# Kernel optimization log

Hardware: AMD Instinct MI355X
Metric: run time of the kernel (lower is better)

## Reference

```python
import jax, jax.numpy as jnp
import numpy as np

B, S, DIM = 2, 2048, 1024
HID = 2048          # multiple_of-rounded hidden dim
E, NSH, TOPK = 8, 2, 2


def _ffn(x, w1, w2, w3):
    return (jax.nn.silu(x @ w1.T) * (x @ w3.T)) @ w2.T


def setup_inputs() -> dict:
    key = jax.random.key(0)
    ks = jax.random.split(key, 8)
    sc = 0.02  # init scale for stability
    return {
        "x": jax.random.normal(ks[0], (B, S, DIM), jnp.float32),
        "router_w": jax.random.normal(ks[1], (E, DIM), jnp.float32) * sc,
        "expert_bias": jnp.zeros((E,), jnp.float32),
        "w1": jax.random.normal(ks[2], (E, HID, DIM), jnp.float32) * sc,
        "w3": jax.random.normal(ks[3], (E, HID, DIM), jnp.float32) * sc,
        "w2": jax.random.normal(ks[4], (E, DIM, HID), jnp.float32) * sc,
        "sw1": jax.random.normal(ks[5], (NSH, HID, DIM), jnp.float32) * sc,
        "sw3": jax.random.normal(ks[6], (NSH, HID, DIM), jnp.float32) * sc,
        "sw2": jax.random.normal(ks[7], (NSH, DIM, HID), jnp.float32) * sc,
    }


def reference(x, router_w, expert_bias, w1, w3, w2, sw1, sw3, sw2):
    bs, sl, d = x.shape
    xf = x.reshape(-1, d)  # [T, d]

    # shared experts (always-on)
    shared = jnp.zeros_like(xf)
    for i in range(sw1.shape[0]):
        shared = shared + _ffn(xf, sw1[i], sw2[i], sw3[i])

    # router with aux-free load-balance bias
    logits = xf @ router_w.T + expert_bias  # [T, E]
    rw, sel = jax.lax.top_k(logits, TOPK)   # [T, K]
    rw = jax.nn.softmax(rw.astype(jnp.float32), axis=-1).astype(x.dtype)

    # combine weights per (token, expert): sum of routing weights over topk slots
    onehot = jax.nn.one_hot(sel, E, dtype=x.dtype)        # [T, K, E]
    combine = jnp.einsum('tk,tke->te', rw, onehot)        # [T, E]

    # per-expert FFN accumulated via scan (equivalent to gather-FFN-scatter)
    def body(acc, ew):
        e1, e3, e2, cw = ew  # cw: [T]
        acc = acc + cw[:, None] * _ffn(xf, e1, e2, e3)
        return acc, None

    out, _ = jax.lax.scan(body, jnp.zeros_like(xf), (w1, w3, w2, combine.T))
    out = out + shared
    return out.reshape(bs, sl, -1)
```

## Files before the change

### kernel.cpp

```cpp
#include <hip/hip_runtime.h>
#include <stdint.h>

#define T_TOK 4096
#define DIMD  1024
#define HIDN  2048
#define NEXP  8
#define RMAX  10240
#define RROWS (RMAX + 2 * T_TOK)

typedef float f32x4 __attribute__((ext_vector_type(4)));
typedef short s16x8 __attribute__((ext_vector_type(8)));

__device__ __forceinline__ uint16_t f2bf(float f) {
    uint32_t u = __builtin_bit_cast(uint32_t, f);
    u += 0x7fffu + ((u >> 16) & 1u);
    return (uint16_t)(u >> 16);
}
__device__ __forceinline__ float bf2f(uint32_t h) {
    return __builtin_bit_cast(float, h << 16);
}
__device__ __forceinline__ uint32_t pk2(float a, float b) {
    return (uint32_t)f2bf(a) | ((uint32_t)f2bf(b) << 16);
}
__device__ __forceinline__ int swz(int r, int cbyte) {
    return r * 128 + (cbyte ^ ((r & 7) << 4));
}
__device__ __forceinline__ void gload16(const void* g, void* l) {
    __builtin_amdgcn_global_load_lds(
        (const __attribute__((address_space(1))) void*)g,
        (__attribute__((address_space(3))) void*)l, 16, 0, 0);
}
#define BAR()        asm volatile("s_barrier" ::: "memory")
#define WAIT_VM4()   asm volatile("s_waitcnt vmcnt(4)" ::: "memory")
#define WAIT_VM0()   asm volatile("s_waitcnt vmcnt(0)" ::: "memory")
#define WAIT_LGKM0() asm volatile("s_waitcnt lgkmcnt(0)" ::: "memory")

__device__ __forceinline__ void stage128x64(const uint16_t* gbase, int ldk,
                                            char* lds, int wv, int lane) {
    #pragma unroll
    for (int i = 0; i < 4; ++i) {
        int s = (wv * 4 + i) * 64 + lane;
        int row = s >> 3;
        int cb = ((s & 7) << 4) ^ ((row & 7) << 4);
        gload16(gbase + (size_t)row * ldk + (cb >> 1), lds + ((wv * 4 + i) << 10));
    }
}


struct CvtArgs {
    const float* s[7];
    uint16_t*    d[7];
    int          nq[7];
    int          mode[7];
};

__global__ void cvt_all_kernel(CvtArgs a) {
    int base = blockIdx.x * blockDim.x + threadIdx.x;
    int stride = gridDim.x * blockDim.x;
    #pragma unroll
    for (int seg = 0; seg < 7; ++seg) {
        const float4* sp = (const float4*)a.s[seg];
        uint2* dp = (uint2*)a.d[seg];
        int n = a.nq[seg];
        int mode = a.mode[seg];
        for (int i = base; i < n; i += stride) {
            float4 v = sp[i];
            uint2 o; o.x = pk2(v.x, v.y); o.y = pk2(v.z, v.w);
            int di = i;
            if (mode) {
                int e = i >> 19;
                int rem = i & 524287;
                int nr = rem >> 8;
                int kq = rem & 255;
                int np = ((nr >> 4) << 5) + ((mode == 2) ? 16 : 0) + (nr & 15);
                di = (e << 20) + (np << 8) + kq;
            }
            dp[di] = o;
        }
    }
}

__global__ __launch_bounds__(256)
void router_kernel(const float* __restrict__ x, const float* __restrict__ rw,
                   const float* __restrict__ bias,
                   int* __restrict__ sel, float* __restrict__ wgt,
                   int* __restrict__ cnt) {
    __shared__ float rws[NEXP * DIMD];
    int tid = threadIdx.x;
    for (int i = tid; i < NEXP * DIMD / 4; i += 256)
        ((float4*)rws)[i] = ((const float4*)rw)[i];
    __syncthreads();

    int wid = tid >> 6, lane = tid & 63;
    float b[NEXP];
    #pragma unroll
    for (int e = 0; e < NEXP; ++e) b[e] = bias[e];

    int t0 = (blockIdx.x * 4 + wid) * 8;
    for (int j = 0; j < 8; ++j) {
        int t = t0 + j;
        const float4* xr = (const float4*)(x + (size_t)t * DIMD);
        float p[NEXP] = {};
        #pragma unroll
        for (int c = 0; c < 4; ++c) {
            float4 xv = xr[c * 64 + lane];
            #pragma unroll
            for (int e = 0; e < NEXP; ++e) {
                float4 wv = *(const float4*)(rws + e * DIMD + c * 256 + lane * 4);
                p[e] += xv.x * wv.x + xv.y * wv.y + xv.z * wv.z + xv.w * wv.w;
            }
        }
        #pragma unroll
        for (int off = 32; off >= 1; off >>= 1) {
            #pragma unroll
            for (int e = 0; e < NEXP; ++e) p[e] += __shfl_xor(p[e], off, 64);
        }
        if (lane == 0) {
            #pragma unroll
            for (int e = 0; e < NEXP; ++e) p[e] += b[e];
            float l0 = -1e30f; int i0 = 0;
            #pragma unroll
            for (int e = 0; e < NEXP; ++e) { if (p[e] > l0) { l0 = p[e]; i0 = e; } }
            float l1 = -1e30f; int i1 = 0;
            #pragma unroll
            for (int e = 0; e < NEXP; ++e) { if (e == i0) continue; if (p[e] > l1) { l1 = p[e]; i1 = e; } }
            float e1 = expf(l1 - l0);
            float d = 1.f + e1;
            sel[t * 2] = i0; sel[t * 2 + 1] = i1;
            wgt[t * 2] = 1.f / d; wgt[t * 2 + 1] = e1 / d;
            atomicAdd(&cnt[i0], 1);
            atomicAdd(&cnt[i1], 1);
        }
    }
}

__global__ void offs_kernel(const int* __restrict__ cnt, int* __restrict__ offs) {
    if (threadIdx.x == 0 && blockIdx.x == 0) {
        int o = 0;
        for (int e = 0; e < NEXP; ++e) { offs[e] = o; o += (cnt[e] + 255) & ~255; }
        offs[NEXP] = o;
    }
}

__global__ void assign_kernel(const int* __restrict__ sel, const int* __restrict__ offs,
                              int* __restrict__ fill, int* __restrict__ row_of,
                              int* __restrict__ tok) {
    int i = blockIdx.x * blockDim.x + threadIdx.x;
    if (i < 2 * T_TOK) {
        int e = sel[i];
        int r = offs[e] + atomicAdd(&fill[e], 1);
        row_of[i] = r;
        tok[r] = i >> 1;
    } else if (i < 4 * T_TOK) {
        int j = i - 2 * T_TOK;
        tok[offs[NEXP] + j] = j & (T_TOK - 1);
    }
}

__global__ void combine_kernel(const uint16_t* __restrict__ H2, const int* __restrict__ row_of,
                               const float* __restrict__ wgt, const int* __restrict__ offs,
                               float* __restrict__ out) {
    int t = blockIdx.x;
    int c = threadIdx.x * 8;
    int r0 = row_of[t * 2], r1 = row_of[t * 2 + 1];
    int s0 = offs[NEXP] + t, s1 = s0 + T_TOK;
    float w0 = wgt[t * 2], w1 = wgt[t * 2 + 1];
    uint4 a = *(const uint4*)(H2 + (size_t)r0 * DIMD + c);
    uint4 b = *(const uint4*)(H2 + (size_t)r1 * DIMD + c);
    uint4 u = *(const uint4*)(H2 + (size_t)s0 * DIMD + c);
    uint4 v = *(const uint4*)(H2 + (size_t)s1 * DIMD + c);
    float4 o0, o1;
    o0.x = w0 * bf2f(a.x & 0xffffu) + w1 * bf2f(b.x & 0xffffu) + bf2f(u.x & 0xffffu) + bf2f(v.x & 0xffffu);
    o0.y = w0 * bf2f(a.x >> 16)     + w1 * bf2f(b.x >> 16)     + bf2f(u.x >> 16)     + bf2f(v.x >> 16);
    o0.z = w0 * bf2f(a.y & 0xffffu) + w1 * bf2f(b.y & 0xffffu) + bf2f(u.y & 0xffffu) + bf2f(v.y & 0xffffu);
    o0.w = w0 * bf2f(a.y >> 16)     + w1 * bf2f(b.y >> 16)     + bf2f(u.y >> 16)     + bf2f(v.y >> 16);
    o1.x = w0 * bf2f(a.z & 0xffffu) + w1 * bf2f(b.z & 0xffffu) + bf2f(u.z & 0xffffu) + bf2f(v.z & 0xffffu);
    o1.y = w0 * bf2f(a.z >> 16)     + w1 * bf2f(b.z >> 16)     + bf2f(u.z >> 16)     + bf2f(v.z >> 16);
    o1.z = w0 * bf2f(a.w & 0xffffu) + w1 * bf2f(b.w & 0xffffu) + bf2f(u.w & 0xffffu) + bf2f(v.w & 0xffffu);
    o1.w = w0 * bf2f(a.w >> 16)     + w1 * bf2f(b.w >> 16)     + bf2f(u.w >> 16)     + bf2f(v.w >> 16);
    float* o = out + (size_t)t * DIMD + c;
    *(float4*)o = o0;
    *(float4*)(o + 4) = o1;
}

__global__ __launch_bounds__(512, 2)
void gemm13_8p(const uint16_t* __restrict__ A, const int* __restrict__ tok,
               const uint16_t* __restrict__ W, uint16_t* __restrict__ H,
               const int* __restrict__ offs) {
    constexpr int K = DIMD;
    constexpr int NT = K / 64;
    __shared__ __align__(16) char lds[131072];

    int row0 = blockIdx.y * 256;
    int rsh = row0 - offs[NEXP];
    int e;
    if (rsh >= 0) {
        if (rsh >= 2 * T_TOK) return;
        e = NEXP + (rsh >> 12);
    } else {
        e = 0;
        while (row0 >= offs[e + 1]) ++e;
    }
    const uint16_t* wp = W + (size_t)e * (4096ull * 1024ull);
    int col0 = blockIdx.x * 256;

    int tid = threadIdx.x, lane = tid & 63, wid = tid >> 6;
    int wm = wid >> 2, wn = wid & 3;

    int sslot = (lane & 3) ^ ((tid >> 3) & 3);
    uint32_t aoff[2], boff[2];
    #pragma unroll
    for (int i = 0; i < 2; ++i) {
        int r = i * 128 + (tid >> 2);
        int garow = tok[row0 + r];
        aoff[i] = (uint32_t)garow * K + sslot * 8;
        boff[i] = (uint32_t)(col0 + r) * K + sslot * 8;
    }
    int ldsw = wid * 1024;

    int rslot = (((lane >> 4) ^ ((lane >> 1) & 3)) << 4);
    int aro = (wm * 128 + (lane & 15)) * 64 + rslot;
    int bro = (wn * 64 + (lane & 15)) * 64 + rslot;

    #define STAGE_A(buf, kt, ks) { \
        gload16(A + aoff[0] + (kt) + (ks) * 32, (buf) + (ks) * 16384 + ldsw); \
        gload16(A + aoff[1] + (kt) + (ks) * 32, (buf) + (ks) * 16384 + 8192 + ldsw); }
    #define STAGE_B(buf, kt, ks) { \
        gload16(wp + boff[0] + (kt) + (ks) * 32, (buf) + 32768 + (ks) * 16384 + ldsw); \
        gload16(wp + boff[1] + (kt) + (ks) * 32, (buf) + 32768 + (ks) * 16384 + 8192 + ldsw); }

    STAGE_A(lds, 0, 0); STAGE_B(lds, 0, 0);
    STAGE_A(lds, 0, 1); STAGE_B(lds, 0, 1);
    WAIT_VM4();
    BAR();

    f32x4 acc[8][4] = {};

    for (int t = 0; t < NT; ++t) {
        char* cur = lds + (t & 1) * 65536;
        char* nxt = lds + ((t + 1) & 1) * 65536;
        int kt1 = (t + 1) * 64;
        bool pre = (t + 1 < NT);
        s16x8 av[4], bv[4], av2[4];

        #pragma unroll
        for (int f = 0; f < 4; ++f) av[f] = *(const s16x8*)(cur + aro + f * 1024);
        #pragma unroll
        for (int f = 0; f < 4; ++f) bv[f] = *(const s16x8*)(cur + 32768 + bro + f * 1024);
        if (pre) STAGE_A(nxt, kt1, 0);
        BAR(); WAIT_LGKM0();
        __builtin_amdgcn_s_setprio(1);
        #pragma unroll
        for (int j = 0; j < 4; ++j)
            #pragma unroll
            for (int i = 0; i < 4; ++i)
                acc[i][j] = __builtin_amdgcn_mfma_f32_16x16x32_bf16(av[i], bv[j], acc[i][j], 0, 0, 0);
        __builtin_amdgcn_s_setprio(0);
        BAR();

        #pragma unroll
        for (int f = 0; f < 4; ++f) av2[f] = *(const s16x8*)(cur + aro + (f + 4) * 1024);
        if (pre) STAGE_B(nxt, kt1, 0);
        BAR(); WAIT_LGKM0();
        __builtin_amdgcn_s_setprio(1);
        #pragma unroll
        for (int j = 0; j < 4; ++j)
            #pragma unroll
            for (int i = 0; i < 4; ++i)
                acc[i + 4][j] = __builtin_amdgcn_mfma_f32_16x16x32_bf16(av2[i], bv[j], acc[i + 4][j], 0, 0, 0);
        __builtin_amdgcn_s_setprio(0);
        if (pre) { WAIT_VM4(); } else { WAIT_VM0(); }
        BAR();

        #pragma unroll
        for (int f = 0; f < 4; ++f) av[f] = *(const s16x8*)(cur + 16384 + aro + f * 1024);
        #pragma unroll
        for (int f = 0; f < 4; ++f) bv[f] = *(const s16x8*)(cur + 32768 + 16384 + bro + f * 1024);
        if (pre) STAGE_A(nxt, kt1, 1);
        BAR(); WAIT_LGKM0();
        __builtin_amdgcn_s_setprio(1);
        #pragma unroll
        for (int j = 0; j < 4; ++j)
            #pragma unroll
            for (int i = 0; i < 4; ++i)
                acc[i][j] = __builtin_amdgcn_mfma_f32_16x16x32_bf16(av[i], bv[j], acc[i][j], 0, 0, 0);
        __builtin_amdgcn_s_setprio(0);
        BAR();

        #pragma unroll
        for (int f = 0; f < 4; ++f) av2[f] = *(const s16x8*)(cur + 16384 + aro + (f + 4) * 1024);
        if (pre) STAGE_B(nxt, kt1, 1);
        BAR(); WAIT_LGKM0();
        __builtin_amdgcn_s_setprio(1);
        #pragma unroll
        for (int j = 0; j < 4; ++j)
            #pragma unroll
            for (int i = 0; i < 4; ++i)
                acc[i + 4][j] = __builtin_amdgcn_mfma_f32_16x16x32_bf16(av2[i], bv[j], acc[i + 4][j], 0, 0, 0);
        __builtin_amdgcn_s_setprio(0);
        if (pre) WAIT_VM4();
        BAR();
    }
    #undef STAGE_A
    #undef STAGE_B

    #pragma unroll
    for (int i = 0; i < 8; ++i) {
        int row = row0 + wm * 128 + i * 16 + ((lane >> 4) << 2);
        #pragma unroll
        for (int m = 0; m < 2; ++m) {
            int hc = ((col0 + wn * 64) >> 1) + m * 16 + (lane & 15);
            #pragma unroll
            for (int rg = 0; rg < 4; ++rg) {
                float a1 = acc[i][2 * m][rg];
                float a3 = acc[i][2 * m + 1][rg];
                float hv = (a1 / (1.f + __expf(-a1))) * a3;
                H[(size_t)(row + rg) * HIDN + hc] = f2bf(hv);
            }
        }
    }
}

__global__ __launch_bounds__(256, 3)
void gemm2_kernel(const uint16_t* __restrict__ Hg,
                  const uint16_t* __restrict__ W2, uint16_t* __restrict__ H2,
                  const int* __restrict__ offs) {
    __shared__ __align__(16) char lds[32768];
    char* As = lds;
    char* Bs = lds + 16384;

    const int K = HIDN;
    int row0 = blockIdx.y * 128;
    int rsh = row0 - offs[NEXP];
    int e;
    if (rsh >= 0) {
        if (rsh >= 2 * T_TOK) return;
        e = NEXP + (rsh >> 12);
    } else {
        e = 0;
        while (row0 >= offs[e + 1]) ++e;
    }
    const uint16_t* b2 = W2 + (size_t)e * DIMD * HIDN;
    int col0 = blockIdx.x * 128;

    int tid = threadIdx.x, lane = tid & 63;
    int wv = tid >> 6, wm = wv >> 1, wn = wv & 1;

    f32x4 acc[4][4] = {};

    for (int kt = 0; kt < K; kt += 64) {
        __syncthreads();
        stage128x64(Hg + (size_t)row0 * K + kt, K, As, wv, lane);
        stage128x64(b2 + (size_t)col0 * K + kt, K, Bs, wv, lane);
        __syncthreads();

        #pragma unroll
        for (int s = 0; s < 2; ++s) {
            int cb = s * 64 + ((lane >> 4) << 4);
            s16x8 av[4];
            #pragma unroll
            for (int i = 0; i < 4; ++i)
                av[i] = *(const s16x8*)(As + swz(wm * 64 + i * 16 + (lane & 15), cb));
            #pragma unroll
            for (int j = 0; j < 4; ++j) {
                s16x8 bv = *(const s16x8*)(Bs + swz(wn * 64 + j * 16 + (lane & 15), cb));
                #pragma unroll
                for (int i = 0; i < 4; ++i)
                    acc[i][j] = __builtin_amdgcn_mfma_f32_16x16x32_bf16(av[i], bv, acc[i][j], 0, 0, 0);
            }
        }
    }

    #pragma unroll
    for (int i = 0; i < 4; ++i) {
        #pragma unroll
        for (int j = 0; j < 4; ++j) {
            #pragma unroll
            for (int rg = 0; rg < 4; ++rg) {
                int row = row0 + wm * 64 + i * 16 + ((lane >> 4) << 2) + rg;
                int col = col0 + wn * 64 + j * 16 + (lane & 15);
                H2[(size_t)row * DIMD + col] = f2bf(acc[i][j][rg]);
            }
        }
    }
}


extern "C" void kernel_launch(void* const* d_in, const int* in_sizes, int n_in,
                              void* d_out, int out_size, void* d_ws, size_t ws_size,
                              hipStream_t stream) {
    const float* x   = (const float*)d_in[0];
    const float* rw  = (const float*)d_in[1];
    const float* eb  = (const float*)d_in[2];
    const float* w1  = (const float*)d_in[3];
    const float* w3  = (const float*)d_in[4];
    const float* w2  = (const float*)d_in[5];
    const float* sw1 = (const float*)d_in[6];
    const float* sw3 = (const float*)d_in[7];
    const float* sw2 = (const float*)d_in[8];
    float* out = (float*)d_out;

    const size_t EW = (size_t)NEXP * HIDN * DIMD;
    const size_t SW = (size_t)2 * HIDN * DIMD;

    char* ws = (char*)d_ws;
    size_t off = 0;
    auto alloc = [&](size_t b) { char* p = ws + off; off = (off + b + 255) & ~(size_t)255; return p; };
    uint16_t* xb    = (uint16_t*)alloc((size_t)T_TOK * DIMD * 2);
    uint16_t* Hg    = (uint16_t*)alloc((size_t)RROWS * HIDN * 2);
    uint16_t* H2    = (uint16_t*)alloc((size_t)RROWS * DIMD * 2);
    uint16_t* w13   = (uint16_t*)alloc((size_t)10 * 4096 * 1024 * 2);
    uint16_t* w2all = (uint16_t*)alloc((EW + SW) * 2);
    int*   sel    = (int*)  alloc(T_TOK * 2 * 4);
    float* wgt    = (float*)alloc(T_TOK * 2 * 4);
    int*   row_of = (int*)  alloc(T_TOK * 2 * 4);
    int*   tok    = (int*)  alloc(RROWS * 4);
    int*   cnt    = (int*)  alloc(64);
    int*   fill   = (int*)  alloc(64);
    int*   offs   = (int*)  alloc(64);

    hipMemsetAsync(cnt, 0, 64, stream);
    hipMemsetAsync(fill, 0, 64, stream);
    hipMemsetAsync(tok, 0, RROWS * 4, stream);

    CvtArgs ca;
    ca.s[0] = w1;  ca.d[0] = w13;                           ca.nq[0] = (int)(EW / 4); ca.mode[0] = 1;
    ca.s[1] = sw1; ca.d[1] = w13 + (size_t)8 * 4096 * 1024; ca.nq[1] = (int)(SW / 4); ca.mode[1] = 1;
    ca.s[2] = w3;  ca.d[2] = w13;                           ca.nq[2] = (int)(EW / 4); ca.mode[2] = 2;
    ca.s[3] = sw3; ca.d[3] = w13 + (size_t)8 * 4096 * 1024; ca.nq[3] = (int)(SW / 4); ca.mode[3] = 2;
    ca.s[4] = w2;  ca.d[4] = w2all;                         ca.nq[4] = (int)(EW / 4); ca.mode[4] = 0;
    ca.s[5] = sw2; ca.d[5] = w2all + EW;                    ca.nq[5] = (int)(SW / 4); ca.mode[5] = 0;
    ca.s[6] = x;   ca.d[6] = xb;                            ca.nq[6] = T_TOK * DIMD / 4; ca.mode[6] = 0;
    cvt_all_kernel<<<2048, 256, 0, stream>>>(ca);

    router_kernel<<<128, 256, 0, stream>>>(x, rw, eb, sel, wgt, cnt);
    offs_kernel<<<1, 1, 0, stream>>>(cnt, offs);
    assign_kernel<<<64, 256, 0, stream>>>(sel, offs, fill, row_of, tok);

    gemm13_8p<<<dim3(16, RROWS / 256), 512, 0, stream>>>(xb, tok, w13, Hg, offs);
    gemm2_kernel<<<dim3(DIMD / 128, RROWS / 128), 256, 0, stream>>>(Hg, w2all, H2, offs);

    combine_kernel<<<T_TOK, 128, 0, stream>>>(H2, row_of, wgt, offs, out);
}
```

Measured before the change: 484.5 us.

## Double-buffer gemm2 LDS tiles with async prefetch and MFMA priority

Rewrites the down-projection GEMM so that the next K tile is loaded into a second LDS buffer while MFMAs run on the current one. Each tile is split into two 32-wide K halves, with staggered vmcnt waits and a new swizzle layout. The goal is to hide global-to-LDS load latency, which the old load, sync, compute loop exposed on every iteration. In exchange the kernel uses 64KB of LDS and launch bounds drop from 3 blocks per CU to 2, which lowers occupancy.

```diff
diff --git a/kernel.cpp b/kernel.cpp
--- a/kernel.cpp
+++ b/kernel.cpp
@@ -22,9 +22,6 @@
 __device__ __forceinline__ uint32_t pk2(float a, float b) {
     return (uint32_t)f2bf(a) | ((uint32_t)f2bf(b) << 16);
 }
-__device__ __forceinline__ int swz(int r, int cbyte) {
-    return r * 128 + (cbyte ^ ((r & 7) << 4));
-}
 __device__ __forceinline__ void gload16(const void* g, void* l) {
     __builtin_amdgcn_global_load_lds(
         (const __attribute__((address_space(1))) void*)g,
@@ -34,17 +31,6 @@
 #define WAIT_VM4()   asm volatile("s_waitcnt vmcnt(4)" ::: "memory")
 #define WAIT_VM0()   asm volatile("s_waitcnt vmcnt(0)" ::: "memory")
 #define WAIT_LGKM0() asm volatile("s_waitcnt lgkmcnt(0)" ::: "memory")
-
-__device__ __forceinline__ void stage128x64(const uint16_t* gbase, int ldk,
-                                            char* lds, int wv, int lane) {
-    #pragma unroll
-    for (int i = 0; i < 4; ++i) {
-        int s = (wv * 4 + i) * 64 + lane;
-        int row = s >> 3;
-        int cb = ((s & 7) << 4) ^ ((row & 7) << 4);
-        gload16(gbase + (size_t)row * ldk + (cb >> 1), lds + ((wv * 4 + i) << 10));
-    }
-}
 
 
 struct CvtArgs {
@@ -321,15 +307,14 @@
     }
 }
 
-__global__ __launch_bounds__(256, 3)
-void gemm2_kernel(const uint16_t* __restrict__ Hg,
-                  const uint16_t* __restrict__ W2, uint16_t* __restrict__ H2,
-                  const int* __restrict__ offs) {
-    __shared__ __align__(16) char lds[32768];
-    char* As = lds;
-    char* Bs = lds + 16384;
-
-    const int K = HIDN;
+__global__ __launch_bounds__(256, 2)
+void gemm2_2p(const uint16_t* __restrict__ Hg,
+              const uint16_t* __restrict__ W2, uint16_t* __restrict__ H2,
+              const int* __restrict__ offs) {
+    constexpr int K = HIDN;
+    constexpr int NT = K / 64;
+    __shared__ __align__(16) char lds[65536];
+
     int row0 = blockIdx.y * 128;
     int rsh = row0 - offs[NEXP];
     int e;
@@ -340,36 +325,81 @@
         e = 0;
         while (row0 >= offs[e + 1]) ++e;
     }
-    const uint16_t* b2 = W2 + (size_t)e * DIMD * HIDN;
+    const uint16_t* wp = W2 + (size_t)e * DIMD * HIDN;
     int col0 = blockIdx.x * 128;
 
-    int tid = threadIdx.x, lane = tid & 63;
-    int wv = tid >> 6, wm = wv >> 1, wn = wv & 1;
+    int tid = threadIdx.x, lane = tid & 63, wid = tid >> 6;
+    int wm = wid >> 1, wn = wid & 1;
+
+    int chunk = (tid & 3) ^ ((tid >> 3) & 3);
+    uint32_t aoff[2], boff[2];
+    #pragma unroll
+    for (int p = 0; p < 2; ++p) {
+        int r = p * 64 + (tid >> 2);
+        aoff[p] = (uint32_t)(row0 + r) * K + chunk * 8;
+        boff[p] = (uint32_t)(col0 + r) * K + chunk * 8;
+    }
+    int ldsw = wid * 1024;
+
+    int rslot = (((lane >> 4) ^ ((lane >> 1) & 3)) << 4);
+    int aro = (wm * 64 + (lane & 15)) * 64 + rslot;
+    int bro = (wn * 64 + (lane & 15)) * 64 + rslot + 16384;
+
+    #define STG_A2(buf, kt, ks) { \
+        gload16(Hg + aoff[0] + (kt) + (ks) * 32, (buf) + (ks) * 8192 + ldsw); \
+        gload16(Hg + aoff[1] + (kt) + (ks) * 32, (buf) + (ks) * 8192 + 4096 + ldsw); }
+    #define STG_B2(buf, kt, ks) { \
+        gload16(wp + boff[0] + (kt) + (ks) * 32, (buf) + 16384 + (ks) * 8192 + ldsw); \
+        gload16(wp + boff[1] + (kt) + (ks) * 32, (buf) + 16384 + (ks) * 8192 + 4096 + ldsw); }
+
+    STG_A2(lds, 0, 0); STG_B2(lds, 0, 0);
+    STG_A2(lds, 0, 1); STG_B2(lds, 0, 1);
+    WAIT_VM4();
+    BAR();
 
     f32x4 acc[4][4] = {};
 
-    for (int kt = 0; kt < K; kt += 64) {
-        __syncthreads();
-        stage128x64(Hg + (size_t)row0 * K + kt, K, As, wv, lane);
-        stage128x64(b2 + (size_t)col0 * K + kt, K, Bs, wv, lane);
-        __syncthreads();
-
-        #pragma unroll
-        for (int s = 0; s < 2; ++s) {
-            int cb = s * 64 + ((lane >> 4) << 4);
-            s16x8 av[4];
-            #pragma unroll
-            for (int i = 0; i < 4; ++i)
-                av[i] = *(const s16x8*)(As + swz(wm * 64 + i * 16 + (lane & 15), cb));
-            #pragma unroll
-            for (int j = 0; j < 4; ++j) {
-                s16x8 bv = *(const s16x8*)(Bs + swz(wn * 64 + j * 16 + (lane & 15), cb));
-                #pragma unroll
-                for (int i = 0; i < 4; ++i)
-                    acc[i][j] = __builtin_amdgcn_mfma_f32_16x16x32_bf16(av[i], bv, acc[i][j], 0, 0, 0);
-            }
-        }
-    }
+    for (int t = 0; t < NT; ++t) {
+        char* cur = lds + (t & 1) * 32768;
+        char* nxt = lds + ((t + 1) & 1) * 32768;
+        int kt1 = (t + 1) * 64;
+        bool pre = (t + 1 < NT);
+        s16x8 av[4], bv[4];
+
+        #pragma unroll
+        for (int f = 0; f < 4; ++f) av[f] = *(const s16x8*)(cur + aro + f * 1024);
+        #pragma unroll
+        for (int f = 0; f < 4; ++f) bv[f] = *(const s16x8*)(cur + bro + f * 1024);
+        if (pre) { STG_A2(nxt, kt1, 0); STG_B2(nxt, kt1, 0); }
+        BAR(); WAIT_LGKM0();
+        __builtin_amdgcn_s_setprio(1);
+        #pragma unroll
+        for (int j = 0; j < 4; ++j)
+            #pragma unroll
+            for (int i = 0; i < 4; ++i)
+                acc[i][j] = __builtin_amdgcn_mfma_f32_16x16x32_bf16(av[i], bv[j], acc[i][j], 0, 0, 0);
+        __builtin_amdgcn_s_setprio(0);
+        if (pre) { WAIT_VM4(); } else { WAIT_VM0(); }
+        BAR();
+
+        #pragma unroll
+        for (int f = 0; f < 4; ++f) av[f] = *(const s16x8*)(cur + 8192 + aro + f * 1024);
+        #pragma unroll
+        for (int f = 0; f < 4; ++f) bv[f] = *(const s16x8*)(cur + 8192 + bro + f * 1024);
+        if (pre) { STG_A2(nxt, kt1, 1); STG_B2(nxt, kt1, 1); }
+        BAR(); WAIT_LGKM0();
+        __builtin_amdgcn_s_setprio(1);
+        #pragma unroll
+        for (int j = 0; j < 4; ++j)
+            #pragma unroll
+            for (int i = 0; i < 4; ++i)
+                acc[i][j] = __builtin_amdgcn_mfma_f32_16x16x32_bf16(av[i], bv[j], acc[i][j], 0, 0, 0);
+        __builtin_amdgcn_s_setprio(0);
+        if (pre) WAIT_VM4();
+        BAR();
+    }
+    #undef STG_A2
+    #undef STG_B2
 
     #pragma unroll
     for (int i = 0; i < 4; ++i) {
@@ -438,7 +468,7 @@
     assign_kernel<<<64, 256, 0, stream>>>(sel, offs, fill, row_of, tok);
 
     gemm13_8p<<<dim3(16, RROWS / 256), 512, 0, stream>>>(xb, tok, w13, Hg, offs);
-    gemm2_kernel<<<dim3(DIMD / 128, RROWS / 128), 256, 0, stream>>>(Hg, w2all, H2, offs);
+    gemm2_2p<<<dim3(DIMD / 128, RROWS / 128), 256, 0, stream>>>(Hg, w2all, H2, offs);
 
     combine_kernel<<<T_TOK, 128, 0, stream>>>(H2, row_of, wgt, offs, out);
 }
```

Result: no change. 483.6 us (-0.2%).
